# Kernel tuning notes

Hardware: AMD Instinct MI355X
Metric: run time of the kernel (lower is better)

## Reference

```python
import jax, jax.numpy as jnp
import numpy as np

TAU = 2.0      # LIF time constant
EPS = 1e-5     # BatchNorm eps
ALPHA = 4.0    # sigmoid surrogate-gradient sharpness (spikingjelly default)

@jax.custom_vjp
def _spike(x):
    return (x >= 0.0).astype(x.dtype)

def _spike_fwd(x):
    return _spike(x), x

def _spike_bwd(x, g):
    s = jax.nn.sigmoid(ALPHA * x)
    return (g * ALPHA * s * (1.0 - s),)

_spike.defvjp(_spike_fwd, _spike_bwd)

def lif(x_seq, v_th=1.0):
    # Multi-step LIF with hard reset to 0, detach_reset=True, v[0]=0.
    # x_seq: (T, ...) ; scan over T.
    def step(v, x):
        v = v + (x - v) / TAU
        s = _spike(v - v_th)
        v = v * (1.0 - jax.lax.stop_gradient(s))  # detach_reset
        return v, s
    _, s_seq = jax.lax.scan(step, jnp.zeros_like(x_seq[0]), x_seq)
    return s_seq

def bn(x, gamma, beta, mean, var):
    # inference-mode BatchNorm2d on (T,B,C,H,W), params (C,)
    sh = (1, 1, -1, 1, 1)
    scale = gamma.reshape(sh) * jax.lax.rsqrt(var.reshape(sh) + EPS)
    return (x - mean.reshape(sh)) * scale + beta.reshape(sh)

def conv1x1(x, w):
    # 1x1 conv == channel matmul; x: (T,B,C,H,W), w: (Cout,Cin)
    return jnp.einsum('tbchw,dc->tbdhw', x, w)

def setup_inputs() -> dict:
    key = jax.random.key(0)
    ks = jax.random.split(key, 24)
    T, B, C, H, W = 4, 32, 384, 16, 16
    d = {}
    d['x'] = jax.random.normal(ks[0], (T, B, C, H, W), jnp.float32)
    for i, p in enumerate(['q', 'k', 'v']):
        base = 1 + 5 * i
        d[p + '_w'] = jax.random.normal(ks[base], (C, C), jnp.float32) * 0.05
        d[p + '_gamma'] = jax.random.uniform(ks[base + 1], (C,), jnp.float32) + 0.5
        d[p + '_beta'] = jax.random.normal(ks[base + 2], (C,), jnp.float32) * 0.1
        d[p + '_mean'] = jax.random.normal(ks[base + 3], (C,), jnp.float32) * 0.1
        d[p + '_var'] = jax.random.uniform(ks[base + 4], (C,), jnp.float32) + 0.5
    d['proj_w'] = jax.random.normal(ks[16], (C, C), jnp.float32) * 0.05
    d['proj_b'] = jax.random.normal(ks[17], (C,), jnp.float32) * 0.1
    d['proj_gamma'] = jax.random.uniform(ks[18], (C,), jnp.float32) + 0.5
    d['proj_beta'] = jax.random.normal(ks[19], (C,), jnp.float32) * 0.1
    d['proj_mean'] = jax.random.normal(ks[20], (C,), jnp.float32) * 0.1
    d['proj_var'] = jax.random.uniform(ks[21], (C,), jnp.float32) + 0.5
    d['num_heads'] = 8
    return d

def reference(x, q_w, q_gamma, q_beta, q_mean, q_var,
              k_w, k_gamma, k_beta, k_mean, k_var,
              v_w, v_gamma, v_beta, v_mean, v_var,
              proj_w, proj_b, proj_gamma, proj_beta, proj_mean, proj_var,
              num_heads):
    T, B, C, H, W = x.shape
    N = H * W
    Ch = C // num_heads
    identity = x
    xs = lif(x)  # shortcut_lif

    def branch(w, g, b, m, var_):
        o = lif(bn(conv1x1(xs, w), g, b, m, var_))  # (T,B,C,H,W), binary spikes
        # flatten(3).transpose(-1,-2).reshape(T,B,N,h,Ch).permute -> (T,B,h,N,Ch)
        return o.reshape(T, B, num_heads, Ch, N).transpose(0, 1, 2, 4, 3)

    q = branch(q_w, q_gamma, q_beta, q_mean, q_var)
    k = branch(k_w, k_gamma, k_beta, k_mean, k_var)
    v = branch(v_w, v_gamma, v_beta, v_mean, v_var)

    kv = (k * v).sum(axis=3, keepdims=True)      # (T,B,h,1,Ch) linear-attn reduce over N
    kv = lif(kv, v_th=0.5)                       # talking_heads_lif
    y = q * kv                                   # (T,B,h,N,Ch)
    y = y.transpose(0, 1, 2, 4, 3).reshape(T, B, C, H, W)
    y = conv1x1(y, proj_w) + proj_b.reshape(1, 1, -1, 1, 1)
    y = bn(y, proj_gamma, proj_beta, proj_mean, proj_var)
    return (y + identity, v)
```

## Files before the change

kernel.cpp:

```cpp
#include <hip/hip_runtime.h>

typedef unsigned short u16;
typedef unsigned char u8;
typedef signed char i8;
typedef int i32x4 __attribute__((ext_vector_type(4)));
typedef int i32x16 __attribute__((ext_vector_type(16)));
typedef float f32x4 __attribute__((ext_vector_type(4)));
typedef unsigned u32x4 __attribute__((ext_vector_type(4)));
typedef u8 u8x16 __attribute__((ext_vector_type(16)));

#define CHS 2097152L

__device__ __forceinline__ void gload16(const void* g, void* l) {
    __builtin_amdgcn_global_load_lds(
        (const __attribute__((address_space(1))) void*)g,
        (__attribute__((address_space(3))) void*)l, 16, 0, 0);
}

__global__ __launch_bounds__(256) void prep(const float* __restrict__ X, u8* __restrict__ Xt,
    const float* __restrict__ qw, const float* __restrict__ kw,
    const float* __restrict__ vw, const float* __restrict__ pw,
    i8* __restrict__ Wq, float* __restrict__ Sc, float* __restrict__ KVraw) {
    const int bid = blockIdx.x;
    if (bid < 768) {
        __shared__ __attribute__((aligned(16))) u8 s2[4][32][136];
        const int c0 = (bid % 3) * 128;
        const int n0 = ((bid / 3) & 7) * 32;
        const int b = bid / 24;
        const int n_l = threadIdx.x & 31, cg = threadIdx.x >> 5;
        for (int jj = 0; jj < 16; jj++) {
            int c_l = cg + jj * 8;
            float vm = 0.f;
            #pragma unroll
            for (int t = 0; t < 4; t++) {
                float xv = __builtin_nontemporal_load(&X[(((long)t * 32 + b) * 384 + c0 + c_l) * 256 + n0 + n_l]);
                vm += (xv - vm) * 0.5f;
                u8 sp = 0;
                if (vm >= 1.0f) { sp = 1; vm = 0.f; }
                s2[t][n_l][c_l] = sp;
            }
        }
        __syncthreads();
        const int c16 = (threadIdx.x & 7) << 4;
        const int n = (threadIdx.x >> 3) & 31;
        const int cglob = c0 + c16;
        const int ch = cglob >> 6, off = cglob & 63;
        #pragma unroll
        for (int t = 0; t < 4; t++) {
            u8x16 v = *(const u8x16*)&s2[t][n][c16];
            *(u8x16*)&Xt[(long)ch * CHS + ((long)(b * 256 + n0 + n) * 4 + t) * 64 + off] = v;
        }
    } else {
        const int wv = bid - 768;
        const int w = threadIdx.x >> 6, lane = threadIdx.x & 63;
        const int r = wv * 4 + w;
        const int m = r / 384, d = r - m * 384;
        const float* srcs[4] = {qw, kw, vw, pw};
        const float* row = srcs[m] + (long)d * 384;
        float a[6]; float mx = 0.f;
        #pragma unroll
        for (int jj = 0; jj < 6; jj++) { a[jj] = row[lane + (jj << 6)]; mx = fmaxf(mx, fabsf(a[jj])); }
        #pragma unroll
        for (int off = 1; off < 64; off <<= 1) mx = fmaxf(mx, __shfl_xor(mx, off));
        float scale = mx * (1.f / 127.f);
        float sinv = mx > 0.f ? 127.f / mx : 0.f;
        if (lane == 0) Sc[r] = scale;
        i8* dstb = Wq + (long)(m == 3 ? 9 : m * 3) * 147456 + (long)d * 64;
        #pragma unroll
        for (int jj = 0; jj < 6; jj++) {
            float x = a[jj] * sinv;
            float q1 = rintf(x);         float r1 = x - q1;
            float q2 = rintf(r1 * 128.f); float r2 = r1 * 128.f - q2;
            float q3 = rintf(r2 * 128.f);
            int co = jj * 24576 + lane;
            dstb[co] = (i8)(int)q1;
            dstb[147456 + co] = (i8)(int)q2;
            if (m != 3) dstb[2 * 147456 + co] = (i8)(int)q3;
        }
        const int idx = wv * 256 + threadIdx.x;
        if (idx < 49152) KVraw[idx] = 0.f;
    }
}

template<int NL>
__device__ __forceinline__ void gemm_i8(const u8* __restrict__ A, const i8* __restrict__ B,
                                        char* lds8, int m0, int n0, i32x16 (&acc)[NL][2]) {
    const int tid = threadIdx.x, l = tid & 63, w = tid >> 6;
    const int wm = (w & 1) << 6, wn = (w >> 1) << 5;
    const int col = l & 31, kg = l >> 5;
    const int rA = tid >> 2, sl = tid & 3;
    const int cs = (sl ^ ((rA >> 1) & 3)) << 4;
    const u8* Ap = A + (long)(m0 + rA) * 64 + cs;
    const i8* Bp = B + (long)(n0 + rA) * 64 + cs;
    const int BUFSZ = (2 + NL) * 4096;
    char* dst = lds8 + tid * 16;

    {
        gload16(Ap, dst);
        gload16(Ap + 4096, dst + 4096);
        #pragma unroll
        for (int p = 0; p < NL; p++)
            gload16(Bp + p * 147456, dst + 8192 + p * 4096);
    }
    __syncthreads();
    for (int ck = 0; ck < 6; ck++) {
        const int cur = ck & 1;
        if (ck < 5) {
            char* d = dst + (cur ^ 1) * BUFSZ;
            gload16(Ap + (ck + 1) * CHS, d);
            gload16(Ap + (ck + 1) * CHS + 4096, d + 4096);
            #pragma unroll
            for (int p = 0; p < NL; p++)
                gload16(Bp + p * 147456 + (ck + 1) * 24576, d + 8192 + p * 4096);
        }
        char* base = lds8 + cur * BUFSZ;
        #pragma unroll
        for (int c = 0; c < 2; c++) {
            i32x4 af[2];
            #pragma unroll
            for (int i = 0; i < 2; i++) {
                int ra = wm + (i << 5) + col;
                int sa = ((2 * c + kg) ^ ((ra >> 1) & 3)) << 4;
                af[i] = *(const i32x4*)(base + ra * 64 + sa);
            }
            int rb = wn + col;
            int sb = ((2 * c + kg) ^ ((rb >> 1) & 3)) << 4;
            #pragma unroll
            for (int p = 0; p < NL; p++) {
                i32x4 bf = *(const i32x4*)(base + 8192 + p * 4096 + rb * 64 + sb);
                #pragma unroll
                for (int i = 0; i < 2; i++)
                    acc[p][i] = __builtin_amdgcn_mfma_i32_32x32x32_i8(af[i], bf, acc[p][i], 0, 0, 0);
            }
        }
        __syncthreads();
    }
}

__global__ __launch_bounds__(256, 4) void k2(
    const u8* __restrict__ Xt, const i8* __restrict__ Wq, const float* __restrict__ Sc,
    const float* __restrict__ g0, const float* __restrict__ b0, const float* __restrict__ m0_, const float* __restrict__ v0_,
    const float* __restrict__ g1, const float* __restrict__ b1, const float* __restrict__ m1_, const float* __restrict__ v1_,
    const float* __restrict__ g2, const float* __restrict__ b2, const float* __restrict__ m2_, const float* __restrict__ v2_,
    u8* __restrict__ oq, u8* __restrict__ ok, u8* __restrict__ ov, float* __restrict__ out1)
{
    __shared__ __attribute__((aligned(16))) char lds8[40960];
    const int bid = blockIdx.x;
    const int xcd = bid & 7, bi = bid >> 3;
    const int mt = (bi / 18) * 8 + xcd;
    const int sub = bi % 18;
    const int m0 = mt * 128, d0 = (sub % 6) * 64, br = sub / 6;
    const float* G  = br == 0 ? g0  : (br == 1 ? g1  : g2);
    const float* Be = br == 0 ? b0  : (br == 1 ? b1  : b2);
    const float* Mu = br == 0 ? m0_ : (br == 1 ? m1_ : m2_);
    const float* Va = br == 0 ? v0_ : (br == 1 ? v1_ : v2_);

    i32x16 acc[3][2];
    #pragma unroll
    for (int p = 0; p < 3; p++)
        #pragma unroll
        for (int i = 0; i < 2; i++)
            #pragma unroll
            for (int r = 0; r < 16; r++) acc[p][i][r] = 0;
    gemm_i8<3>(Xt, Wq + (long)br * 3 * 147456, lds8, m0, d0, acc);

    const int tid = threadIdx.x, l = tid & 63, w = tid >> 6;
    const int wm = (w & 1) << 6, wn = (w >> 1) << 5;
    const int col = l & 31;
    const int d = d0 + wn + col;
    const float scb = G[d] / sqrtf(Va[d] + 1e-5f);
    const float mu = Mu[d], be = Be[d];
    const float wsc = Sc[br * 384 + d];
    u8* tile8 = (u8*)lds8;
    const float c1 = 0.0078125f, c2 = 6.103515625e-05f;
    #pragma unroll
    for (int i = 0; i < 2; i++)
        #pragma unroll
        for (int q = 0; q < 4; q++) {
            float vm = 0.f;
            int mb = wm + (i << 5) + (q << 3) + ((l >> 5) << 2);
            #pragma unroll
            for (int t = 0; t < 4; t++) {
                int reg = q * 4 + t;
                float f = (float)acc[0][i][reg] + (float)acc[1][i][reg] * c1
                        + (float)acc[2][i][reg] * c2;
                float bn = (f * wsc - mu) * scb + be;
                vm += (bn - vm) * 0.5f;
                u8 s = 0;
                if (vm >= 1.0f) { s = 1; vm = 0.f; }
                tile8[(mb + t) * 80 + wn + col] = s;
            }
        }
    __syncthreads();
    u8* Out8 = br == 0 ? oq : (br == 1 ? ok : ov);
    const long rbase = (long)(d0 >> 6) * CHS + (long)m0 * 64;
    u32x4 w0 = *(const u32x4*)&tile8[(tid >> 2) * 80 + ((tid & 3) << 4)];
    u32x4 w1 = *(const u32x4*)&tile8[(64 + (tid >> 2)) * 80 + ((tid & 3) << 4)];
    *(u32x4*)(Out8 + rbase + tid * 16) = w0;
    *(u32x4*)(Out8 + rbase + 4096 + tid * 16) = w1;
    if (br == 2) {
        const int b = m0 >> 10, n_base = (m0 >> 2) & 255;
        const int dl4 = (tid & 15) << 2;
        const int d2 = d0 + dl4;
        const int h = d2 / 48, chn = d2 - h * 48;
        #pragma unroll
        for (int q = 0; q < 8; q++) {
            int mlq = (tid >> 4) + (q << 4);
            int t = mlq & 3, n = n_base + (mlq >> 2);
            f32x4 v;
            #pragma unroll
            for (int r = 0; r < 4; r++) v[r] = tile8[mlq * 80 + dl4 + r] ? 1.0f : 0.f;
            long gi = ((((long)t * 32 + b) * 8 + h) * 256 + n) * 48 + chn;
            __builtin_nontemporal_store(v, (f32x4*)&out1[gi]);
        }
    }
}

__global__ __launch_bounds__(384) void k3a(const u8* __restrict__ Ks, const u8* __restrict__ Vs,
                                           float* __restrict__ kv_raw) {
    const int b = blockIdx.y, nc = blockIdx.x;
    const int d4 = threadIdx.x * 4, t = threadIdx.y;
    const long cbase = (long)(d4 >> 6) * CHS + (d4 & 63);
    int cnt0 = 0, cnt1 = 0, cnt2 = 0, cnt3 = 0;
    for (int nl = 0; nl < 32; nl++) {
        const long row = ((long)b * 256 + nc * 32 + nl) * 4 + t;
        uchar4 kk = *(const uchar4*)&Ks[cbase + row * 64];
        uchar4 vv = *(const uchar4*)&Vs[cbase + row * 64];
        cnt0 += (kk.x & vv.x); cnt1 += (kk.y & vv.y);
        cnt2 += (kk.z & vv.z); cnt3 += (kk.w & vv.w);
    }
    float* dst = &kv_raw[((long)t * 32 + b) * 384 + d4];
    atomicAdd(dst + 0, (float)cnt0);
    atomicAdd(dst + 1, (float)cnt1);
    atomicAdd(dst + 2, (float)cnt2);
    atomicAdd(dst + 3, (float)cnt3);
}

__global__ __launch_bounds__(256) void k3c(const u8* __restrict__ Qs, const float* __restrict__ kv_raw,
                                           u8* __restrict__ Y) {
    __shared__ __attribute__((aligned(16))) u8 kvs_s[4][64];
    const int tid = threadIdx.x;
    const int u0 = blockIdx.x << 8;
    const int ch = u0 >> 17;
    const int mb = (u0 >> 2) & 32767;
    const int b = mb >> 10;
    if (tid < 64) {
        float vm = 0.f;
        #pragma unroll
        for (int t = 0; t < 4; t++) {
            vm += (kv_raw[((long)t * 32 + b) * 384 + ch * 64 + tid] - vm) * 0.5f;
            u8 sp = 0;
            if (vm >= 0.5f) { sp = 1; vm = 0.f; }
            kvs_s[t][tid] = sp;
        }
    }
    __syncthreads();
    const int m = mb + (tid >> 2), off16 = (tid & 3) << 4;
    const int t = m & 3;
    const long ca = (long)ch * CHS + (long)m * 64 + off16;
    u32x4 q = *(const u32x4*)(Qs + ca);
    u32x4 kvv = *(const u32x4*)&kvs_s[t][off16];
    u32x4 y = q & kvv;
    *(u32x4*)(Y + ca) = y;
}

__global__ __launch_bounds__(256, 4) void k4(
    const u8* __restrict__ Y, const i8* __restrict__ Pq, const float* __restrict__ Scp,
    const float* __restrict__ PB, const float* __restrict__ PG, const float* __restrict__ PBe,
    const float* __restrict__ PM, const float* __restrict__ PV,
    const float* __restrict__ X, float* __restrict__ O)
{
    __shared__ __attribute__((aligned(16))) char lds8[33792];
    const int bid = blockIdx.x;
    const int xcd = bid & 7, bi = bid >> 3;
    const int mt = (bi / 6) * 8 + xcd;
    const int m0 = mt * 128, e0 = (bi % 6) * 64;
    i32x16 acc[2][2];
    #pragma unroll
    for (int p = 0; p < 2; p++)
        #pragma unroll
        for (int i = 0; i < 2; i++)
            #pragma unroll
            for (int r = 0; r < 16; r++) acc[p][i][r] = 0;
    gemm_i8<2>(Y, Pq, lds8, m0, e0, acc);

    const int tid = threadIdx.x, l = tid & 63, w = tid >> 6;
    const int wm = (w & 1) << 6, wn = (w >> 1) << 5;
    const int col = l & 31;
    const int e = e0 + wn + col;
    const float scb = PG[e] / sqrtf(PV[e] + 1e-5f);
    const float mu = PM[e], be = PBe[e], pbb = PB[e];
    const float wsc = Scp[e];
    float* smemf = (float*)lds8;
    const float c1 = 0.0078125f;
    #pragma unroll
    for (int i = 0; i < 2; i++)
        #pragma unroll
        for (int q = 0; q < 4; q++)
            #pragma unroll
            for (int t = 0; t < 4; t++) {
                int reg = q * 4 + t;
                float f = (float)acc[0][i][reg] + (float)acc[1][i][reg] * c1;
                float z = (f * wsc + pbb - mu) * scb + be;
                int m = wm + (i << 5) + (q << 3) + ((l >> 5) << 2) + t;
                smemf[(wn + col) * 132 + m] = z;
            }
    __syncthreads();
    const int b = m0 >> 10, n_base = (m0 >> 2) & 255;
    const int n_l = tid & 31;
    #pragma unroll
    for (int ei = 0; ei < 8; ei++) {
        int e_l = (tid >> 5) + (ei << 3);
        f32x4 v = *(const f32x4*)&smemf[e_l * 132 + (n_l << 2)];
        #pragma unroll
        for (int t = 0; t < 4; t++) {
            long gi = (((long)t * 32 + b) * 384 + e0 + e_l) * 256 + n_base + n_l;
            float xv = __builtin_nontemporal_load(&X[gi]);
            __builtin_nontemporal_store(v[t] + xv, &O[gi]);
        }
    }
}

extern "C" void kernel_launch(void* const* d_in, const int* in_sizes, int n_in,
                              void* d_out, int out_size, void* d_ws, size_t ws_size,
                              hipStream_t stream) {
    (void)in_sizes; (void)n_in; (void)out_size; (void)ws_size;
    const float* x   = (const float*)d_in[0];
    const float* qw  = (const float*)d_in[1];
    const float* qg  = (const float*)d_in[2];
    const float* qb  = (const float*)d_in[3];
    const float* qm  = (const float*)d_in[4];
    const float* qv  = (const float*)d_in[5];
    const float* kw  = (const float*)d_in[6];
    const float* kg  = (const float*)d_in[7];
    const float* kb  = (const float*)d_in[8];
    const float* km  = (const float*)d_in[9];
    const float* kv  = (const float*)d_in[10];
    const float* vw  = (const float*)d_in[11];
    const float* vg  = (const float*)d_in[12];
    const float* vb  = (const float*)d_in[13];
    const float* vm  = (const float*)d_in[14];
    const float* vv  = (const float*)d_in[15];
    const float* pw  = (const float*)d_in[16];
    const float* pb  = (const float*)d_in[17];
    const float* pg  = (const float*)d_in[18];
    const float* pbe = (const float*)d_in[19];
    const float* pm  = (const float*)d_in[20];
    const float* pv  = (const float*)d_in[21];

    float* out0 = (float*)d_out;
    float* out1 = out0 + 12582912;
    char*  ob   = (char*)d_out;
    u8*    Qs8  = (u8*)ob;
    u8*    Xt8  = (u8*)(ob + 12582912);
    char*  ws   = (char*)d_ws;
    u8*    Ks8  = (u8*)ws;
    u8*    Vs8  = (u8*)ws + 12582912;
    u8*    Yb8  = (u8*)ws;
    float* KVraw = (float*)(ws + 25165824);
    i8*    Wq    = (i8*)(ws + 25411584);
    float* Sc    = (float*)(ws + 27033600);

    hipLaunchKernelGGL(prep, dim3(1152), dim3(256), 0, stream, x, Xt8, qw, kw, vw, pw, Wq, Sc, KVraw);
    hipLaunchKernelGGL(k2, dim3(4608), dim3(256), 0, stream,
                       Xt8, Wq, Sc,
                       qg, qb, qm, qv,
                       kg, kb, km, kv,
                       vg, vb, vm, vv,
                       Qs8, Ks8, Vs8, out1);
    hipLaunchKernelGGL(k3a, dim3(8, 32), dim3(96, 4), 0, stream, Ks8, Vs8, KVraw);
    hipLaunchKernelGGL(k3c, dim3(3072), dim3(256), 0, stream, Qs8, KVraw, Yb8);
    hipLaunchKernelGGL(k4, dim3(768 * 2), dim3(256), 0, stream,
                       Yb8, Wq + 9 * 147456L, Sc + 3 * 384, pb, pg, pbe, pm, pv, x, out0);
}
```

Before: 263.3 us.

## Fuse talking-heads LIF and Q masking into projection GEMM; vectorize prep loads

Measured after the change: 259.6 us. About the same (-1.4%).

```diff
diff --git a/kernel.cpp b/kernel.cpp
--- a/kernel.cpp
+++ b/kernel.cpp
@@ -27,17 +27,23 @@
         const int c0 = (bid % 3) * 128;
         const int n0 = ((bid / 3) & 7) * 32;
         const int b = bid / 24;
-        const int n_l = threadIdx.x & 31, cg = threadIdx.x >> 5;
-        for (int jj = 0; jj < 16; jj++) {
-            int c_l = cg + jj * 8;
-            float vm = 0.f;
+        const int n4 = (threadIdx.x & 7) << 2;
+        const int cl0 = threadIdx.x >> 3;
+        #pragma unroll
+        for (int pass = 0; pass < 4; pass++) {
+            const int c_l = cl0 + (pass << 5);
+            f32x4 vm = {0.f, 0.f, 0.f, 0.f};
             #pragma unroll
             for (int t = 0; t < 4; t++) {
-                float xv = __builtin_nontemporal_load(&X[(((long)t * 32 + b) * 384 + c0 + c_l) * 256 + n0 + n_l]);
-                vm += (xv - vm) * 0.5f;
-                u8 sp = 0;
-                if (vm >= 1.0f) { sp = 1; vm = 0.f; }
-                s2[t][n_l][c_l] = sp;
+                f32x4 xv = __builtin_nontemporal_load(
+                    (const f32x4*)&X[(((long)t * 32 + b) * 384 + c0 + c_l) * 256 + n0 + n4]);
+                #pragma unroll
+                for (int e = 0; e < 4; e++) {
+                    vm[e] += (xv[e] - vm[e]) * 0.5f;
+                    u8 sp = 0;
+                    if (vm[e] >= 1.0f) { sp = 1; vm[e] = 0.f; }
+                    s2[t][n4 + e][c_l] = sp;
+                }
             }
         }
         __syncthreads();
@@ -236,45 +242,34 @@
     atomicAdd(dst + 3, (float)cnt3);
 }
 
-__global__ __launch_bounds__(256) void k3c(const u8* __restrict__ Qs, const float* __restrict__ kv_raw,
-                                           u8* __restrict__ Y) {
-    __shared__ __attribute__((aligned(16))) u8 kvs_s[4][64];
-    const int tid = threadIdx.x;
-    const int u0 = blockIdx.x << 8;
-    const int ch = u0 >> 17;
-    const int mb = (u0 >> 2) & 32767;
-    const int b = mb >> 10;
-    if (tid < 64) {
-        float vm = 0.f;
-        #pragma unroll
-        for (int t = 0; t < 4; t++) {
-            vm += (kv_raw[((long)t * 32 + b) * 384 + ch * 64 + tid] - vm) * 0.5f;
-            u8 sp = 0;
-            if (vm >= 0.5f) { sp = 1; vm = 0.f; }
-            kvs_s[t][tid] = sp;
-        }
-    }
-    __syncthreads();
-    const int m = mb + (tid >> 2), off16 = (tid & 3) << 4;
-    const int t = m & 3;
-    const long ca = (long)ch * CHS + (long)m * 64 + off16;
-    u32x4 q = *(const u32x4*)(Qs + ca);
-    u32x4 kvv = *(const u32x4*)&kvs_s[t][off16];
-    u32x4 y = q & kvv;
-    *(u32x4*)(Y + ca) = y;
-}
-
 __global__ __launch_bounds__(256, 4) void k4(
-    const u8* __restrict__ Y, const i8* __restrict__ Pq, const float* __restrict__ Scp,
+    const u8* __restrict__ Qs, const float* __restrict__ kv_raw,
+    const i8* __restrict__ Pq, const float* __restrict__ Scp,
     const float* __restrict__ PB, const float* __restrict__ PG, const float* __restrict__ PBe,
     const float* __restrict__ PM, const float* __restrict__ PV,
     const float* __restrict__ X, float* __restrict__ O)
 {
-    __shared__ __attribute__((aligned(16))) char lds8[33792];
+    __shared__ __attribute__((aligned(16))) char lds8[35328];
+    u8* kvs_s = (u8*)(lds8 + 33792);
     const int bid = blockIdx.x;
     const int xcd = bid & 7, bi = bid >> 3;
     const int mt = (bi / 6) * 8 + xcd;
     const int m0 = mt * 128, e0 = (bi % 6) * 64;
+    const int tid = threadIdx.x;
+    const int b = m0 >> 10;
+
+    for (int dd = tid; dd < 384; dd += 256) {
+        float vm = 0.f;
+        #pragma unroll
+        for (int t = 0; t < 4; t++) {
+            vm += (kv_raw[((long)t * 32 + b) * 384 + dd] - vm) * 0.5f;
+            u8 sp = 0;
+            if (vm >= 0.5f) { sp = 1; vm = 0.f; }
+            kvs_s[t * 384 + dd] = sp;
+        }
+    }
+    __syncthreads();
+
     i32x16 acc[2][2];
     #pragma unroll
     for (int p = 0; p < 2; p++)
@@ -282,11 +277,61 @@
         for (int i = 0; i < 2; i++)
             #pragma unroll
             for (int r = 0; r < 16; r++) acc[p][i][r] = 0;
-    gemm_i8<2>(Y, Pq, lds8, m0, e0, acc);
-
-    const int tid = threadIdx.x, l = tid & 63, w = tid >> 6;
+    const int l = tid & 63, w = tid >> 6;
     const int wm = (w & 1) << 6, wn = (w >> 1) << 5;
-    const int col = l & 31;
+    const int col = l & 31, kg = l >> 5;
+    const int rA = tid >> 2, sl = tid & 3;
+    const int cs = (sl ^ ((rA >> 1) & 3)) << 4;
+    const int tA = rA & 3;
+    const u8* Ap = Qs + (long)(m0 + rA) * 64 + cs;
+    const i8* Bp = Pq + (long)(e0 + rA) * 64 + cs;
+    const int BUFSZ = 16384;
+    char* dst = lds8 + tid * 16;
+    {
+        u32x4 mk = *(const u32x4*)&kvs_s[tA * 384 + cs];
+        u32x4 q0 = *(const u32x4*)(Ap);
+        u32x4 q1 = *(const u32x4*)(Ap + 4096);
+        gload16(Bp, dst + 8192);
+        gload16(Bp + 147456, dst + 12288);
+        *(u32x4*)dst = q0 & mk;
+        *(u32x4*)(dst + 4096) = q1 & mk;
+    }
+    __syncthreads();
+    for (int ck = 0; ck < 6; ck++) {
+        const int cur = ck & 1;
+        if (ck < 5) {
+            char* dn = dst + (cur ^ 1) * BUFSZ;
+            u32x4 mk = *(const u32x4*)&kvs_s[tA * 384 + (ck + 1) * 64 + cs];
+            u32x4 q0 = *(const u32x4*)(Ap + (ck + 1) * CHS);
+            u32x4 q1 = *(const u32x4*)(Ap + (ck + 1) * CHS + 4096);
+            gload16(Bp + (ck + 1) * 24576, dn + 8192);
+            gload16(Bp + 147456 + (ck + 1) * 24576, dn + 12288);
+            *(u32x4*)dn = q0 & mk;
+            *(u32x4*)(dn + 4096) = q1 & mk;
+        }
+        char* base = lds8 + cur * BUFSZ;
+        #pragma unroll
+        for (int c = 0; c < 2; c++) {
+            i32x4 af[2];
+            #pragma unroll
+            for (int i = 0; i < 2; i++) {
+                int ra = wm + (i << 5) + col;
+                int sa = ((2 * c + kg) ^ ((ra >> 1) & 3)) << 4;
+                af[i] = *(const i32x4*)(base + ra * 64 + sa);
+            }
+            int rb = wn + col;
+            int sb = ((2 * c + kg) ^ ((rb >> 1) & 3)) << 4;
+            #pragma unroll
+            for (int p = 0; p < 2; p++) {
+                i32x4 bf = *(const i32x4*)(base + 8192 + p * 4096 + rb * 64 + sb);
+                #pragma unroll
+                for (int i = 0; i < 2; i++)
+                    acc[p][i] = __builtin_amdgcn_mfma_i32_32x32x32_i8(af[i], bf, acc[p][i], 0, 0, 0);
+            }
+        }
+        __syncthreads();
+    }
+
     const int e = e0 + wn + col;
     const float scb = PG[e] / sqrtf(PV[e] + 1e-5f);
     const float mu = PM[e], be = PBe[e], pbb = PB[e];
@@ -306,7 +351,7 @@
                 smemf[(wn + col) * 132 + m] = z;
             }
     __syncthreads();
-    const int b = m0 >> 10, n_base = (m0 >> 2) & 255;
+    const int n_base = (m0 >> 2) & 255;
     const int n_l = tid & 31;
     #pragma unroll
     for (int ei = 0; ei < 8; ei++) {
@@ -356,7 +401,6 @@
     char*  ws   = (char*)d_ws;
     u8*    Ks8  = (u8*)ws;
     u8*    Vs8  = (u8*)ws + 12582912;
-    u8*    Yb8  = (u8*)ws;
     float* KVraw = (float*)(ws + 25165824);
     i8*    Wq    = (i8*)(ws + 25411584);
     float* Sc    = (float*)(ws + 27033600);
@@ -369,7 +413,6 @@
                        vg, vb, vm, vv,
                        Qs8, Ks8, Vs8, out1);
     hipLaunchKernelGGL(k3a, dim3(8, 32), dim3(96, 4), 0, stream, Ks8, Vs8, KVraw);
-    hipLaunchKernelGGL(k3c, dim3(3072), dim3(256), 0, stream, Qs8, KVraw, Yb8);
-    hipLaunchKernelGGL(k4, dim3(768 * 2), dim3(256), 0, stream,
-                       Yb8, Wq + 9 * 147456L, Sc + 3 * 384, pb, pg, pbe, pm, pv, x, out0);
-}
+    hipLaunchKernelGGL(k4, dim3(1536), dim3(256), 0, stream,
+                       Qs8, KVraw, Wq + 9 * 147456L, Sc + 3 * 384, pb, pg, pbe, pm, pv, x, out0);
+}
```
